# Performance work log

Measured on AMD Instinct MI355X. Metric: run time of the kernel, lower is better.

Reference implementation:

```python
import jax, jax.numpy as jnp
import numpy as np
import itertools

EPSILON = 1e-6
OUT_SIZE = 4096
IN_SIZE = 4096
RANK = 2  # in_rank + len(out_shape)
REGION = np.array([16.0, 16.0], dtype=np.float32)
PRIMES = np.array([2, 3], dtype=np.int64)  # first RANK primes from the buffer
# floor/ceil combinations, same order as itertools.product([True, False], repeat=RANK)
FLOOR_MASK = np.array([[int(b) for b in bools] for bools in itertools.product([True, False], repeat=RANK)], dtype=bool)  # (2**RANK, RANK)


def generate_integer_tuples(means, rr_u, g_u, rng_sizes, region):
    # means: (b, k, RANK); rr_u/g_u: uniform(0,1) samples (b, k, radd/gadd, RANK)
    b, k, rank = means.shape
    m = jax.lax.stop_gradient(means)  # torch uses means.data
    mexp = m[:, :, None, :]
    # all floor/ceil corner combinations of the continuous index tuple
    neigh = jnp.where(FLOOR_MASK[None, None, :, :], jnp.floor(mexp), jnp.ceil(mexp)).astype(jnp.int64)
    # uniform samples over the whole index space
    g_ints = jnp.floor(g_u * (1.0 - EPSILON) * rng_sizes).astype(jnp.int64)
    # uniform samples from a small window around round(means)
    mr = jnp.round(mexp)
    lower = mr - region * 0.5
    upper = mr + region * 0.5
    lower = jnp.where(lower < 0.0, 0.0, lower)
    lower = jnp.where(upper > rng_sizes, rng_sizes - region, lower)
    rr_ints = (rr_u * (1.0 - EPSILON) * region + lower).astype(jnp.int64)
    ints = jnp.concatenate([neigh, g_ints, rr_ints], axis=2)  # (b, k, 2**RANK+gadd+radd, RANK)
    return ints.reshape(b, -1, rank)


def duplicates(tuples):
    # tuples: (b, n, r) int64 -> bool mask (b, n) marking all-but-first occurrences
    b, n, r = tuples.shape
    unique = jnp.prod((tuples + 1) ** PRIMES[:r], axis=2)  # prime-power hash
    sort_idx = jnp.argsort(unique, axis=1)
    sorted_v = jnp.take_along_axis(unique, sort_idx, axis=1)
    unsort_idx = jnp.argsort(sort_idx, axis=1)
    mask = jnp.concatenate(
        [jnp.zeros((b, 1), dtype=bool), sorted_v[:, 1:] == sorted_v[:, :-1]], axis=1)
    return jnp.take_along_axis(mask, unsort_idx, axis=1)


def densities(points, means, sigmas):
    # unnormalized diagonal-MVN pdf: exp(-0.5 * sum_r (p_r - m_r)^2 / (eps + sigma_r))
    # expanded quadratic form via einsum to avoid the (b, n, k, r) intermediate
    inv = 1.0 / (EPSILON + sigmas)                                   # (b, k, r)
    a = jnp.einsum('bnr,bkr->bnk', points * points, inv)
    bt = jnp.einsum('bnr,bkr->bnk', points, means * inv)
    c = jnp.sum(means * means * inv, axis=-1)[:, None, :]
    return jnp.exp(-0.5 * (a - 2.0 * bt + c))                        # (b, n, k)


def setup_inputs() -> dict:
    key = jax.random.key(0)
    ks = jax.random.split(key, 7)
    b, k, gadd, radd = 4, 256, 64, 64
    rng = jnp.array([OUT_SIZE, IN_SIZE], dtype=jnp.float32)
    x = jax.random.normal(ks[0], (b, IN_SIZE), dtype=jnp.float32)
    means = jax.random.uniform(ks[1], (b, k, RANK), dtype=jnp.float32) * (rng - 1.0)
    sigmas = (jax.random.uniform(ks[2], (b, k, RANK), dtype=jnp.float32) * 2.0 + 0.5) * (rng / 64.0)
    values = jax.random.normal(ks[3], (b, k), dtype=jnp.float32)
    bias = jax.random.normal(ks[4], (OUT_SIZE,), dtype=jnp.float32)
    rr_u = jax.random.uniform(ks[5], (b, k, radd, RANK), dtype=jnp.float32)
    g_u = jax.random.uniform(ks[6], (b, k, gadd, RANK), dtype=jnp.float32)
    return {"x": x, "means": means, "sigmas": sigmas, "values": values,
            "bias": bias, "rr_u": rr_u, "g_u": g_u}


def reference(x, means, sigmas, values, bias, rr_u, g_u):
    b, in_size = x.shape
    rng_sizes = jnp.array([OUT_SIZE, in_size], dtype=jnp.float32)
    region = jnp.asarray(REGION)
    indices = jax.lax.stop_gradient(
        generate_integer_tuples(means, rr_u, g_u, rng_sizes, region))  # (b, n, 2)
    dups = duplicates(indices)                                        # (b, n) bool
    props = densities(indices.astype(jnp.float32), means, sigmas)     # (b, n, k)
    props = jnp.where(dups[:, :, None], 0.0, props)                   # zero duplicates
    props = props / props.sum(axis=1, keepdims=True)
    weights = jnp.einsum('bnk,bk->bn', props, values)                 # per-index weight
    out_idx = indices[:, :, 0]  # output coordinate (len(out_shape)=1)
    in_idx = indices[:, :, 1]   # input coordinate (in_rank=1)
    gathered = jnp.take_along_axis(x, in_idx, axis=1)                 # (b, n)
    barange = jnp.arange(b)[:, None]
    y = jnp.zeros((b, OUT_SIZE), dtype=x.dtype).at[barange, out_idx].add(weights * gathered)
    return y + bias[None, :]
```

## Files before the change

kernel.cpp:

```cpp
#include <hip/hip_runtime.h>
#include <cstdint>

#define BATCH 4
#define KCOMP 256
#define GADD 64
#define RADD 64
#define PPK 132
#define NPB (KCOMP * PPK)
#define NTOT (BATCH * NPB)
#define OUTS 4096
#define INS 4096
#define TBITS 16
#define TSIZE (1 << TBITS)

#define TPB_A 528
#define NEG_HALF_LOG2E (-0.72134752044448170f)

#define KEYS_BYTES  ((size_t)BATCH * TSIZE * 8)
#define DENOM_BYTES ((size_t)BATCH * KCOMP * 4)
#define VALS_BYTES  ((size_t)BATCH * TSIZE * 4)
#define PTS_BYTES   ((size_t)NTOT * 4)

__device__ __forceinline__ unsigned long long point_hash(long long t0, long long t1) {
    unsigned long long a = (unsigned long long)((t0 + 1) * (t0 + 1));
    unsigned long long b = (unsigned long long)((t1 + 1) * (t1 + 1) * (t1 + 1));
    return a * b;
}

__device__ __forceinline__ unsigned int slot_of(unsigned long long h) {
    return (unsigned int)((h * 0x9E3779B97F4A7C15ull) >> (64 - TBITS));
}

__global__ void k_init_y(const float* __restrict__ bias, float* __restrict__ y) {
    int i = blockIdx.x * blockDim.x + threadIdx.x;
    if (i < BATCH * OUTS) y[i] = bias[i & (OUTS - 1)];
}

__global__ void k_gen(const float* __restrict__ means,
                      const float* __restrict__ rr_u,
                      const float* __restrict__ g_u,
                      uint32_t* __restrict__ pts,
                      unsigned long long* __restrict__ keys,
                      unsigned int* __restrict__ vals) {
    int n = blockIdx.x * blockDim.x + threadIdx.x;
    if (n >= NTOT) return;
    int b = n / NPB;
    int loc = n - b * NPB;
    int k = loc / PPK;
    int j = loc - k * PPK;

    const float* mp = means + (size_t)(b * KCOMP + k) * 2;
    double m0 = (double)mp[0], m1 = (double)mp[1];
    long long t0, t1;
    if (j < 4) {
        t0 = (long long)((j < 2) ? floor(m0) : ceil(m0));
        t1 = (long long)(((j & 1) == 0) ? floor(m1) : ceil(m1));
    } else if (j < 4 + GADD) {
        int gi = j - 4;
        const float* gp = g_u + ((size_t)((b * KCOMP + k) * GADD) + gi) * 2;
        t0 = (long long)floor((double)gp[0] * (1.0 - 1e-6) * 4096.0);
        t1 = (long long)floor((double)gp[1] * (1.0 - 1e-6) * 4096.0);
    } else {
        int ri = j - 4 - GADD;
        const float* rp = rr_u + ((size_t)((b * KCOMP + k) * RADD) + ri) * 2;
        double mr0 = rint(m0), mr1 = rint(m1);
        double lo0 = mr0 - 8.0;
        if (lo0 < 0.0) lo0 = 0.0;
        if (mr0 + 8.0 > 4096.0) lo0 = 4080.0;
        double lo1 = mr1 - 8.0;
        if (lo1 < 0.0) lo1 = 0.0;
        if (mr1 + 8.0 > 4096.0) lo1 = 4080.0;
        t0 = (long long)((double)rp[0] * (1.0 - 1e-6) * 16.0 + lo0);
        t1 = (long long)((double)rp[1] * (1.0 - 1e-6) * 16.0 + lo1);
    }

    pts[n] = (uint32_t)t0 | ((uint32_t)t1 << 12);

    unsigned long long h = point_hash(t0, t1);
    unsigned long long* kb = keys + (size_t)b * TSIZE;
    unsigned int* vb = vals + (size_t)b * TSIZE;
    unsigned int s = slot_of(h);
    for (;;) {
        unsigned long long prev = atomicCAS(&kb[s], 0ull, h);
        if (prev == 0ull || prev == h) {
            atomicMin(&vb[s], (unsigned int)loc);
            break;
        }
        s = (s + 1) & (TSIZE - 1);
    }
}

__global__ void k_denomA(const float* __restrict__ means,
                         const float* __restrict__ sigmas,
                         uint32_t* __restrict__ pts,
                         const unsigned long long* __restrict__ keys,
                         const unsigned int* __restrict__ vals,
                         float* __restrict__ denom) {
    __shared__ float2 spt[64];
    int bid = blockIdx.x;
    int b = bid / TPB_A;
    int tloc = bid - b * TPB_A;
    int t = threadIdx.x;
    int loc = tloc * 64 + t;

    {
        uint32_t p = pts[(size_t)b * NPB + loc];
        long long t0 = (long long)(p & 0xFFFu);
        long long t1 = (long long)((p >> 12) & 0xFFFu);
        unsigned long long h = point_hash(t0, t1);
        const unsigned long long* kb = keys + (size_t)b * TSIZE;
        const unsigned int* vb = vals + (size_t)b * TSIZE;
        unsigned int s = slot_of(h);
        for (;;) {
            if (kb[s] == h) break;
            s = (s + 1) & (TSIZE - 1);
        }
        if (vb[s] != (unsigned int)loc) {
            pts[(size_t)b * NPB + loc] = p | 0x80000000u;
            spt[t] = make_float2(1.0e9f, 0.0f);
        } else {
            spt[t] = make_float2((float)t0, (float)t1);
        }
    }
    __syncthreads();

    float m0[4], m1[4], i0[4], i1[4], acc[4];
#pragma unroll
    for (int q = 0; q < 4; ++q) {
        int bk = b * KCOMP + t + 64 * q;
        m0[q] = means[bk * 2];
        m1[q] = means[bk * 2 + 1];
        i0[q] = NEG_HALF_LOG2E / (1e-6f + sigmas[bk * 2]);
        i1[q] = NEG_HALF_LOG2E / (1e-6f + sigmas[bk * 2 + 1]);
        acc[q] = 0.0f;
    }
#pragma unroll 8
    for (int j = 0; j < 64; ++j) {
        float2 p = spt[j];
#pragma unroll
        for (int q = 0; q < 4; ++q) {
            float dx = p.x - m0[q], dy = p.y - m1[q];
            float e2 = dx * dx * i0[q] + dy * dy * i1[q];
            acc[q] += exp2f(e2);
        }
    }
#pragma unroll
    for (int q = 0; q < 4; ++q)
        atomicAdd(&denom[b * KCOMP + t + 64 * q], acc[q]);
}

__global__ void k_scatterB(const float* __restrict__ means,
                           const float* __restrict__ sigmas,
                           const float* __restrict__ values,
                           const float* __restrict__ denom,
                           const float* __restrict__ x,
                           const uint32_t* __restrict__ pts,
                           float* __restrict__ y) {
    __shared__ float4 prm[KCOMP];
    __shared__ float cf[KCOMP];
    int bid = blockIdx.x;
    int b = bid / TPB_A;
    int tloc = bid - b * TPB_A;
    int t = threadIdx.x;

#pragma unroll
    for (int q = 0; q < 4; ++q) {
        int k = t + 64 * q;
        int bk = b * KCOMP + k;
        float i0 = NEG_HALF_LOG2E / (1e-6f + sigmas[bk * 2]);
        float i1 = NEG_HALF_LOG2E / (1e-6f + sigmas[bk * 2 + 1]);
        prm[k] = make_float4(means[bk * 2], means[bk * 2 + 1], i0, i1);
        cf[k] = values[bk] / denom[bk];
    }
    __syncthreads();

    int loc = tloc * 64 + t;
    uint32_t p = pts[(size_t)b * NPB + loc];
    if (p & 0x80000000u) return;

    float p0 = (float)(p & 0xFFFu);
    float p1 = (float)((p >> 12) & 0xFFFu);
    float w = 0.0f;
#pragma unroll 8
    for (int q = 0; q < KCOMP; ++q) {
        float4 pr = prm[q];
        float dx = p0 - pr.x, dy = p1 - pr.y;
        float e2 = dx * dx * pr.z + dy * dy * pr.w;
        w = fmaf(exp2f(e2), cf[q], w);
    }
    int out_idx = (int)(p & 0xFFFu);
    int in_idx = (int)((p >> 12) & 0xFFFu);
    float val = w * x[(size_t)b * INS + in_idx];
    atomicAdd(&y[(size_t)b * OUTS + out_idx], val);
}

extern "C" void kernel_launch(void* const* d_in, const int* in_sizes, int n_in,
                              void* d_out, int out_size, void* d_ws, size_t ws_size,
                              hipStream_t stream) {
    const float* x      = (const float*)d_in[0];
    const float* means  = (const float*)d_in[1];
    const float* sigmas = (const float*)d_in[2];
    const float* values = (const float*)d_in[3];
    const float* bias   = (const float*)d_in[4];
    const float* rr_u   = (const float*)d_in[5];
    const float* g_u    = (const float*)d_in[6];
    float* y = (float*)d_out;

    uint8_t* w = (uint8_t*)d_ws;
    unsigned long long* keys = (unsigned long long*)w;
    float* denom = (float*)(w + KEYS_BYTES);
    unsigned int* vals = (unsigned int*)(w + KEYS_BYTES + DENOM_BYTES);
    uint32_t* pts = (uint32_t*)(w + KEYS_BYTES + DENOM_BYTES + VALS_BYTES);

    hipMemsetAsync(keys, 0x00, KEYS_BYTES + DENOM_BYTES, stream);
    hipMemsetAsync(vals, 0xFF, VALS_BYTES, stream);

    hipLaunchKernelGGL(k_init_y, dim3((BATCH * OUTS + 255) / 256), dim3(256), 0, stream,
                       bias, y);
    hipLaunchKernelGGL(k_gen, dim3((NTOT + 255) / 256), dim3(256), 0, stream,
                       means, rr_u, g_u, pts, keys, vals);
    hipLaunchKernelGGL(k_denomA, dim3(BATCH * TPB_A), dim3(64), 0, stream,
                       means, sigmas, pts, keys, vals, denom);
    hipLaunchKernelGGL(k_scatterB, dim3(BATCH * TPB_A), dim3(64), 0, stream,
                       means, sigmas, values, denom, x, pts, y);
}
```

Measured before the change: 145.6 us.

## Fuse memsets into init kernel and retile denom/scatter to 256-thread blocks

Replaces the two hipMemsetAsync calls and the bias-init kernel with one vectorized init kernel that zeroes keys/denom, fills vals with 0xFF and writes bias into y. The denominator and scatter kernels now use 256-thread blocks over 256-point tiles, with one component per thread, so there are four times fewer atomics on denom and fewer blocks overall. Both inner loops are split across four independent accumulators to break the serial add dependency. The trade-off is fewer blocks (528 total), which may leave parts of the GPU idle, and a different floating-point summation order.

Measured after the change: 136.2 us. 6.4% less time.

```diff
diff --git a/kernel.cpp b/kernel.cpp
--- a/kernel.cpp
+++ b/kernel.cpp
@@ -12,8 +12,8 @@
 #define INS 4096
 #define TBITS 16
 #define TSIZE (1 << TBITS)
-
-#define TPB_A 528
+#define TILES 132
+
 #define NEG_HALF_LOG2E (-0.72134752044448170f)
 
 #define KEYS_BYTES  ((size_t)BATCH * TSIZE * 8)
@@ -21,6 +21,11 @@
 #define VALS_BYTES  ((size_t)BATCH * TSIZE * 4)
 #define PTS_BYTES   ((size_t)NTOT * 4)
 
+#define ZERO_U4 131328
+#define FF_U4   65536
+#define Y_F4    4096
+#define INIT_TOT (ZERO_U4 + FF_U4 + Y_F4)
+
 __device__ __forceinline__ unsigned long long point_hash(long long t0, long long t1) {
     unsigned long long a = (unsigned long long)((t0 + 1) * (t0 + 1));
     unsigned long long b = (unsigned long long)((t1 + 1) * (t1 + 1) * (t1 + 1));
@@ -31,9 +36,18 @@
     return (unsigned int)((h * 0x9E3779B97F4A7C15ull) >> (64 - TBITS));
 }
 
-__global__ void k_init_y(const float* __restrict__ bias, float* __restrict__ y) {
+__global__ void k_init(const float* __restrict__ bias, float* __restrict__ y,
+                       uint4* __restrict__ zero_base, uint4* __restrict__ ff_base) {
     int i = blockIdx.x * blockDim.x + threadIdx.x;
-    if (i < BATCH * OUTS) y[i] = bias[i & (OUTS - 1)];
+    if (i < ZERO_U4) {
+        zero_base[i] = make_uint4(0u, 0u, 0u, 0u);
+    } else if (i < ZERO_U4 + FF_U4) {
+        ff_base[i - ZERO_U4] = make_uint4(~0u, ~0u, ~0u, ~0u);
+    } else if (i < INIT_TOT) {
+        int j = i - (ZERO_U4 + FF_U4);
+        float4 bv = ((const float4*)bias)[j & 1023];
+        ((float4*)y)[j] = bv;
+    }
 }
 
 __global__ void k_gen(const float* __restrict__ means,
@@ -96,12 +110,12 @@
                          const unsigned long long* __restrict__ keys,
                          const unsigned int* __restrict__ vals,
                          float* __restrict__ denom) {
-    __shared__ float2 spt[64];
+    __shared__ float2 spt[256];
     int bid = blockIdx.x;
-    int b = bid / TPB_A;
-    int tloc = bid - b * TPB_A;
+    int b = bid / TILES;
+    int tile = bid - b * TILES;
     int t = threadIdx.x;
-    int loc = tloc * 64 + t;
+    int loc = tile * 256 + t;
 
     {
         uint32_t p = pts[(size_t)b * NPB + loc];
@@ -111,10 +125,7 @@
         const unsigned long long* kb = keys + (size_t)b * TSIZE;
         const unsigned int* vb = vals + (size_t)b * TSIZE;
         unsigned int s = slot_of(h);
-        for (;;) {
-            if (kb[s] == h) break;
-            s = (s + 1) & (TSIZE - 1);
-        }
+        while (kb[s] != h) s = (s + 1) & (TSIZE - 1);
         if (vb[s] != (unsigned int)loc) {
             pts[(size_t)b * NPB + loc] = p | 0x80000000u;
             spt[t] = make_float2(1.0e9f, 0.0f);
@@ -124,29 +135,22 @@
     }
     __syncthreads();
 
-    float m0[4], m1[4], i0[4], i1[4], acc[4];
-#pragma unroll
-    for (int q = 0; q < 4; ++q) {
-        int bk = b * KCOMP + t + 64 * q;
-        m0[q] = means[bk * 2];
-        m1[q] = means[bk * 2 + 1];
-        i0[q] = NEG_HALF_LOG2E / (1e-6f + sigmas[bk * 2]);
-        i1[q] = NEG_HALF_LOG2E / (1e-6f + sigmas[bk * 2 + 1]);
-        acc[q] = 0.0f;
-    }
-#pragma unroll 8
-    for (int j = 0; j < 64; ++j) {
-        float2 p = spt[j];
-#pragma unroll
-        for (int q = 0; q < 4; ++q) {
-            float dx = p.x - m0[q], dy = p.y - m1[q];
-            float e2 = dx * dx * i0[q] + dy * dy * i1[q];
-            acc[q] += exp2f(e2);
-        }
-    }
-#pragma unroll
-    for (int q = 0; q < 4; ++q)
-        atomicAdd(&denom[b * KCOMP + t + 64 * q], acc[q]);
+    int bk = b * KCOMP + t;
+    float m0 = means[bk * 2], m1 = means[bk * 2 + 1];
+    float i0 = NEG_HALF_LOG2E / (1e-6f + sigmas[bk * 2]);
+    float i1 = NEG_HALF_LOG2E / (1e-6f + sigmas[bk * 2 + 1]);
+
+    float a0 = 0.0f, a1 = 0.0f, a2 = 0.0f, a3 = 0.0f;
+#pragma unroll 4
+    for (int j = 0; j < 256; j += 4) {
+        float2 q0 = spt[j], q1 = spt[j + 1], q2 = spt[j + 2], q3 = spt[j + 3];
+        float dx, dy;
+        dx = q0.x - m0; dy = q0.y - m1; a0 += exp2f(dx * dx * i0 + dy * dy * i1);
+        dx = q1.x - m0; dy = q1.y - m1; a1 += exp2f(dx * dx * i0 + dy * dy * i1);
+        dx = q2.x - m0; dy = q2.y - m1; a2 += exp2f(dx * dx * i0 + dy * dy * i1);
+        dx = q3.x - m0; dy = q3.y - m1; a3 += exp2f(dx * dx * i0 + dy * dy * i1);
+    }
+    atomicAdd(&denom[bk], (a0 + a1) + (a2 + a3));
 }
 
 __global__ void k_scatterB(const float* __restrict__ means,
@@ -159,39 +163,43 @@
     __shared__ float4 prm[KCOMP];
     __shared__ float cf[KCOMP];
     int bid = blockIdx.x;
-    int b = bid / TPB_A;
-    int tloc = bid - b * TPB_A;
+    int b = bid / TILES;
+    int tile = bid - b * TILES;
     int t = threadIdx.x;
 
-#pragma unroll
-    for (int q = 0; q < 4; ++q) {
-        int k = t + 64 * q;
-        int bk = b * KCOMP + k;
+    {
+        int bk = b * KCOMP + t;
         float i0 = NEG_HALF_LOG2E / (1e-6f + sigmas[bk * 2]);
         float i1 = NEG_HALF_LOG2E / (1e-6f + sigmas[bk * 2 + 1]);
-        prm[k] = make_float4(means[bk * 2], means[bk * 2 + 1], i0, i1);
-        cf[k] = values[bk] / denom[bk];
+        prm[t] = make_float4(means[bk * 2], means[bk * 2 + 1], i0, i1);
+        cf[t] = values[bk] / denom[bk];
     }
     __syncthreads();
 
-    int loc = tloc * 64 + t;
+    int loc = tile * 256 + t;
     uint32_t p = pts[(size_t)b * NPB + loc];
     if (p & 0x80000000u) return;
 
     float p0 = (float)(p & 0xFFFu);
     float p1 = (float)((p >> 12) & 0xFFFu);
-    float w = 0.0f;
-#pragma unroll 8
-    for (int q = 0; q < KCOMP; ++q) {
-        float4 pr = prm[q];
-        float dx = p0 - pr.x, dy = p1 - pr.y;
-        float e2 = dx * dx * pr.z + dy * dy * pr.w;
-        w = fmaf(exp2f(e2), cf[q], w);
-    }
+    float w0 = 0.0f, w1 = 0.0f, w2 = 0.0f, w3 = 0.0f;
+#pragma unroll 4
+    for (int q = 0; q < KCOMP; q += 4) {
+        float4 r0 = prm[q], r1 = prm[q + 1], r2 = prm[q + 2], r3 = prm[q + 3];
+        float dx, dy;
+        dx = p0 - r0.x; dy = p1 - r0.y;
+        w0 = fmaf(exp2f(dx * dx * r0.z + dy * dy * r0.w), cf[q], w0);
+        dx = p0 - r1.x; dy = p1 - r1.y;
+        w1 = fmaf(exp2f(dx * dx * r1.z + dy * dy * r1.w), cf[q + 1], w1);
+        dx = p0 - r2.x; dy = p1 - r2.y;
+        w2 = fmaf(exp2f(dx * dx * r2.z + dy * dy * r2.w), cf[q + 2], w2);
+        dx = p0 - r3.x; dy = p1 - r3.y;
+        w3 = fmaf(exp2f(dx * dx * r3.z + dy * dy * r3.w), cf[q + 3], w3);
+    }
+    float w = (w0 + w1) + (w2 + w3);
     int out_idx = (int)(p & 0xFFFu);
     int in_idx = (int)((p >> 12) & 0xFFFu);
-    float val = w * x[(size_t)b * INS + in_idx];
-    atomicAdd(&y[(size_t)b * OUTS + out_idx], val);
+    atomicAdd(&y[(size_t)b * OUTS + out_idx], w * x[(size_t)b * INS + in_idx]);
 }
 
 extern "C" void kernel_launch(void* const* d_in, const int* in_sizes, int n_in,
@@ -212,15 +220,12 @@
     unsigned int* vals = (unsigned int*)(w + KEYS_BYTES + DENOM_BYTES);
     uint32_t* pts = (uint32_t*)(w + KEYS_BYTES + DENOM_BYTES + VALS_BYTES);
 
-    hipMemsetAsync(keys, 0x00, KEYS_BYTES + DENOM_BYTES, stream);
-    hipMemsetAsync(vals, 0xFF, VALS_BYTES, stream);
-
-    hipLaunchKernelGGL(k_init_y, dim3((BATCH * OUTS + 255) / 256), dim3(256), 0, stream,
-                       bias, y);
+    hipLaunchKernelGGL(k_init, dim3((INIT_TOT + 255) / 256), dim3(256), 0, stream,
+                       bias, y, (uint4*)w, (uint4*)(w + KEYS_BYTES + DENOM_BYTES));
     hipLaunchKernelGGL(k_gen, dim3((NTOT + 255) / 256), dim3(256), 0, stream,
                        means, rr_u, g_u, pts, keys, vals);
-    hipLaunchKernelGGL(k_denomA, dim3(BATCH * TPB_A), dim3(64), 0, stream,
+    hipLaunchKernelGGL(k_denomA, dim3(BATCH * TILES), dim3(256), 0, stream,
                        means, sigmas, pts, keys, vals, denom);
-    hipLaunchKernelGGL(k_scatterB, dim3(BATCH * TPB_A), dim3(64), 0, stream,
+    hipLaunchKernelGGL(k_scatterB, dim3(BATCH * TILES), dim3(256), 0, stream,
                        means, sigmas, values, denom, x, pts, y);
 }
```
